# Optimization experiments

Measured on AMD Instinct MI355X. Metric: run time of the kernel, lower is better.

Reference implementation:

```python
import jax, jax.numpy as jnp
import numpy as np

HIDDEN = 4096
HALF = HIDDEN // 2
NUM_EXPERTS = 64
TOP_K = 8
TEMPERATURE = 1.0


def setup_inputs() -> dict:
    key = jax.random.key(0)
    k_x, k_w1, k_w2 = jax.random.split(key, 3)
    B, S = 4, 4096
    x = jax.random.normal(k_x, (B, S, HIDDEN), dtype=jnp.float32)
    attention_mask = jnp.ones((B, S), dtype=jnp.float32)
    # nn.init.normal_(std=0.02), zero bias
    W1 = 0.02 * jax.random.normal(k_w1, (HIDDEN, HALF), dtype=jnp.float32)
    b1 = jnp.zeros((HALF,), dtype=jnp.float32)
    W2 = 0.02 * jax.random.normal(k_w2, (HALF, NUM_EXPERTS), dtype=jnp.float32)
    b2 = jnp.zeros((NUM_EXPERTS,), dtype=jnp.float32)
    return {"x": x, "attention_mask": attention_mask, "W1": W1, "b1": b1, "W2": W2, "b2": b2}


def reference(x, attention_mask, W1, b1, W2, b2):
    B, S, H = x.shape
    x_flat = x.reshape(-1, H)  # [T, H], T = B*S
    # router MLP (eval mode: dropout is identity, no noise)
    h = jax.nn.gelu(x_flat @ W1 + b1, approximate=False)  # [T, H/2]
    logits = h @ W2 + b2  # [T, E]
    T = logits.shape[0]
    # top-k sparse gating: softmax over selected logits, scatter into dense [T, E]
    top_v, top_i = jax.lax.top_k(logits, TOP_K)  # [T, K]
    top_w = jax.nn.softmax(top_v / TEMPERATURE, axis=-1)  # [T, K]
    weights = jnp.zeros_like(logits).at[jnp.arange(T)[:, None], top_i].set(top_w)
    expert_weights = weights.reshape(B, S, NUM_EXPERTS)
    router_logits = logits.reshape(B, S, NUM_EXPERTS)
    mask = attention_mask[:, :, None].astype(expert_weights.dtype)
    expert_weights = expert_weights * mask
    router_logits = router_logits * mask
    return expert_weights, router_logits
```

## Files before the change

kernel.cpp:

```cpp
#include <hip/hip_runtime.h>
#include <hip/hip_bf16.h>
#include <math.h>

#define HIDDEN 4096
#define HALF   2048
#define NE     64
#define TOPK   8

typedef __attribute__((ext_vector_type(8))) short          short8;
typedef __attribute__((ext_vector_type(4))) float          floatx4;
typedef __attribute__((ext_vector_type(4))) unsigned short ushort4v;

__device__ inline unsigned short bf16_rne(float v) {
    union { float f; unsigned u; } x; x.f = v;
    unsigned r = x.u + 0x7fffu + ((x.u >> 16) & 1u);
    return (unsigned short)(r >> 16);
}
__device__ inline float bf16_to_f(unsigned short b) {
    union { unsigned u; float f; } x; x.u = (unsigned)b << 16;
    return x.f;
}

__device__ inline void hstore(float* p, float v) { *p = v; }
__device__ inline void hstore(__hip_bfloat16* p, float v) { *p = __float2bfloat16(v); }
__device__ inline float hload(const float* p) { return *p; }
__device__ inline float hload(const __hip_bfloat16* p) { return __bfloat162float(*p); }
__device__ inline float ntload(const float* p) { return __builtin_nontemporal_load(p); }
__device__ inline float ntload(const __hip_bfloat16* p) { return __bfloat162float(*p); }

__device__ inline void gl2lds16(const void* g, void* l) {
    __builtin_amdgcn_global_load_lds(
        (const __attribute__((address_space(1))) void*)g,
        (__attribute__((address_space(3))) void*)l, 16, 0, 0);
}

__global__ __launch_bounds__(256) void split_x_k(const float* __restrict__ x,
                                                 unsigned short* __restrict__ hi,
                                                 unsigned short* __restrict__ lo) {
    const size_t blk = (size_t)(gridDim.x - 1 - blockIdx.x);
    const size_t i = (blk * 256 + threadIdx.x) * 4;
    floatx4 v = __builtin_nontemporal_load((const floatx4*)(x + i));
    ushort4v h4, l4;
#pragma unroll
    for (int j = 0; j < 4; ++j) {
        unsigned short hb = bf16_rne(v[j]);
        h4[j] = hb;
        l4[j] = bf16_rne(v[j] - bf16_to_f(hb));
    }
    *(ushort4v*)(hi + i) = h4;
    *(ushort4v*)(lo + i) = l4;
}

__global__ __launch_bounds__(256) void split_wt_k(const float* __restrict__ src,
                                                  unsigned short* __restrict__ wh,
                                                  unsigned short* __restrict__ wl,
                                                  int K, int N) {
    __shared__ float tile[64][65];
    const int tid = threadIdx.x;
    const int bk = blockIdx.x * 64, bn = blockIdx.y * 64;
    const int c4 = (tid & 15) * 4, r = tid >> 4;
#pragma unroll
    for (int rr = 0; rr < 4; ++rr) {
        const int row = r + rr * 16;
        *(float4*)&tile[row][c4] = *(const float4*)&src[(size_t)(bk + row) * N + bn + c4];
    }
    __syncthreads();
#pragma unroll
    for (int rr = 0; rr < 4; ++rr) {
        const int n = r + rr * 16;
        ushort4v h4, l4;
#pragma unroll
        for (int j = 0; j < 4; ++j) {
            float v = tile[c4 + j][n];
            unsigned short hb = bf16_rne(v);
            h4[j] = hb;
            l4[j] = bf16_rne(v - bf16_to_f(hb));
        }
        *(ushort4v*)&wh[(size_t)(bn + n) * K + bk + c4] = h4;
        *(ushort4v*)&wl[(size_t)(bn + n) * K + bk + c4] = l4;
    }
}

__global__ __launch_bounds__(256, 2) void gemm1_gelu_pre(const unsigned short* __restrict__ xh,
                                                         const unsigned short* __restrict__ xl,
                                                         const unsigned short* __restrict__ wh,
                                                         const unsigned short* __restrict__ wl,
                                                         const float* __restrict__ bias1,
                                                         float* __restrict__ h) {
    __shared__ unsigned short Ah[2][128][32];
    __shared__ unsigned short Al[2][128][32];
    __shared__ unsigned short Bh[2][128][32];
    __shared__ unsigned short Bl[2][128][32];

    const int tid = threadIdx.x;
    const int id  = blockIdx.x;
    const int c   = id >> 9;
    const int j   = id & 511;
    const int m0  = ((c << 5) | (j >> 4)) * 128;
    const int N0  = (j & 15) * 128;

    const int wave = tid >> 6, lane = tid & 63;
    const int wm   = (wave & 1) * 64;
    const int wn   = (wave >> 1) * 64;
    const int l15  = lane & 15;
    const int q    = lane >> 4;

    const size_t lrow = (size_t)(lane >> 2);
    const int    lcol = (lane & 3) * 8;
    const unsigned short* gp;
    unsigned short* lp;
    if (wave == 0)      { gp = xh + (m0 + lrow) * HIDDEN + lcol; lp = &Ah[0][0][0]; }
    else if (wave == 1) { gp = xl + (m0 + lrow) * HIDDEN + lcol; lp = &Al[0][0][0]; }
    else if (wave == 2) { gp = wh + (N0 + lrow) * HIDDEN + lcol; lp = &Bh[0][0][0]; }
    else                { gp = wl + (N0 + lrow) * HIDDEN + lcol; lp = &Bl[0][0][0]; }

    float bb[4];
#pragma unroll
    for (int jj = 0; jj < 4; ++jj) bb[jj] = bias1[N0 + wn + jj * 16 + l15];
    asm volatile("s_waitcnt vmcnt(0)" ::: "memory");

    const unsigned aoff = ((unsigned)(wm + l15)) * 64 + ((unsigned)q) * 16;
    const unsigned boff = ((unsigned)(wn + l15)) * 64 + ((unsigned)q) * 16;
    const char* AhB = (const char*)&Ah[0][0][0];
    const char* AlB = (const char*)&Al[0][0][0];
    const char* BhB = (const char*)&Bh[0][0][0];
    const char* BlB = (const char*)&Bl[0][0][0];

    floatx4 acc[4][4];
#pragma unroll
    for (int i = 0; i < 4; ++i)
#pragma unroll
        for (int jj = 0; jj < 4; ++jj) acc[i][jj] = (floatx4)0.f;

#pragma unroll
    for (int s = 0; s < 8; ++s)
        gl2lds16(gp + (size_t)s * 16 * HIDDEN, lp + s * 512);
    gp += 32;

    for (int t = 0; t < 128; ++t) {
        const int cur = t & 1;

        asm volatile("" ::: "memory");
        __builtin_amdgcn_s_barrier();

        if (t < 127) {
            unsigned short* lq = lp + (cur ^ 1) * 4096;
#pragma unroll
            for (int s = 0; s < 8; ++s)
                gl2lds16(gp + (size_t)s * 16 * HIDDEN, lq + s * 512);
            gp += 32;
            asm volatile("s_waitcnt vmcnt(8)" ::: "memory");
        } else {
            asm volatile("s_waitcnt vmcnt(0)" ::: "memory");
        }

        __builtin_amdgcn_s_barrier();
        asm volatile("" ::: "memory");

        const unsigned o = (unsigned)cur * 8192;
        short8 a_hi[4], a_lo[4], b_hi[4], b_lo[4];
#pragma unroll
        for (int tt = 0; tt < 4; ++tt) {
            a_hi[tt] = *(const short8*)(AhB + o + aoff + tt * 1024);
            a_lo[tt] = *(const short8*)(AlB + o + aoff + tt * 1024);
            b_hi[tt] = *(const short8*)(BhB + o + boff + tt * 1024);
            b_lo[tt] = *(const short8*)(BlB + o + boff + tt * 1024);
        }
#pragma unroll
        for (int i = 0; i < 4; ++i)
#pragma unroll
            for (int jj = 0; jj < 4; ++jj) {
                acc[i][jj] = __builtin_amdgcn_mfma_f32_16x16x32_bf16(a_hi[i], b_hi[jj], acc[i][jj], 0, 0, 0);
                acc[i][jj] = __builtin_amdgcn_mfma_f32_16x16x32_bf16(a_lo[i], b_hi[jj], acc[i][jj], 0, 0, 0);
                acc[i][jj] = __builtin_amdgcn_mfma_f32_16x16x32_bf16(a_hi[i], b_lo[jj], acc[i][jj], 0, 0, 0);
            }
    }

#pragma unroll
    for (int jj = 0; jj < 4; ++jj) {
        const int n = N0 + wn + jj * 16 + l15;
#pragma unroll
        for (int i = 0; i < 4; ++i) {
            const int mbase = m0 + wm + i * 16 + q * 4;
#pragma unroll
            for (int r = 0; r < 4; ++r) {
                float v = acc[i][jj][r] + bb[jj];
                float g = 0.5f * v * (1.0f + erff(v * 0.70710678118654752f));
                __builtin_nontemporal_store(g, &h[(size_t)(mbase + r) * HALF + n]);
            }
        }
    }
}

template <typename HT>
__global__ __launch_bounds__(256) void gemm2_topk(const HT* __restrict__ h,
                                                  const float* __restrict__ W2,
                                                  const float* __restrict__ bias2,
                                                  const float* __restrict__ amask,
                                                  float* __restrict__ out, int T) {
    __shared__ float hs[4][HALF];
    __shared__ float red[4][4][NE];
    const int tid = threadIdx.x;
    const size_t r0 = (size_t)blockIdx.x * 4;

    float* hsf = &hs[0][0];
    const HT* hr = h + r0 * HALF;
#pragma unroll
    for (int it = 0; it < 8; ++it) {
        const int i = tid * 4 + it * 1024;
        hsf[i + 0] = ntload(hr + i + 0);
        hsf[i + 1] = ntload(hr + i + 1);
        hsf[i + 2] = ntload(hr + i + 2);
        hsf[i + 3] = ntload(hr + i + 3);
    }
    __syncthreads();

    const int e = tid & 63, qq = tid >> 6;
    float s0 = 0.f, s1 = 0.f, s2 = 0.f, s3 = 0.f;
    const float* w = W2 + e;
    const int kbeg = qq * 512;
    for (int k4 = kbeg; k4 < kbeg + 512; k4 += 4) {
        float4 h0 = *(const float4*)&hs[0][k4];
        float4 h1 = *(const float4*)&hs[1][k4];
        float4 h2 = *(const float4*)&hs[2][k4];
        float4 h3 = *(const float4*)&hs[3][k4];
        float wv;
        wv = w[(size_t)(k4 + 0) * NE];
        s0 = fmaf(h0.x, wv, s0); s1 = fmaf(h1.x, wv, s1); s2 = fmaf(h2.x, wv, s2); s3 = fmaf(h3.x, wv, s3);
        wv = w[(size_t)(k4 + 1) * NE];
        s0 = fmaf(h0.y, wv, s0); s1 = fmaf(h1.y, wv, s1); s2 = fmaf(h2.y, wv, s2); s3 = fmaf(h3.y, wv, s3);
        wv = w[(size_t)(k4 + 2) * NE];
        s0 = fmaf(h0.z, wv, s0); s1 = fmaf(h1.z, wv, s1); s2 = fmaf(h2.z, wv, s2); s3 = fmaf(h3.z, wv, s3);
        wv = w[(size_t)(k4 + 3) * NE];
        s0 = fmaf(h0.w, wv, s0); s1 = fmaf(h1.w, wv, s1); s2 = fmaf(h2.w, wv, s2); s3 = fmaf(h3.w, wv, s3);
    }
    red[qq][0][e] = s0;
    red[qq][1][e] = s1;
    red[qq][2][e] = s2;
    red[qq][3][e] = s3;
    __syncthreads();

    const int wave = tid >> 6, lane = tid & 63;
    const size_t r = r0 + wave;
    const float v = ((red[0][wave][lane] + red[1][wave][lane]) +
                     (red[2][wave][lane] + red[3][wave][lane])) + bias2[lane];
    const float mk = amask[r];

    out[(size_t)T * NE + r * NE + lane] = v * mk;

    bool  sel = false;
    float m0 = 0.f, Z = 0.f;
#pragma unroll
    for (int it = 0; it < TOPK; ++it) {
        float cand = sel ? -INFINITY : v;
        int   idx  = lane;
#pragma unroll
        for (int off = 32; off; off >>= 1) {
            float ov = __shfl_xor(cand, off, 64);
            int   oi = __shfl_xor(idx,  off, 64);
            if (ov > cand || (ov == cand && oi < idx)) { cand = ov; idx = oi; }
        }
        if (it == 0) m0 = cand;
        Z += expf(cand - m0);
        if (lane == idx) sel = true;
    }
    const float wgt = sel ? (expf(v - m0) / Z) : 0.f;
    out[r * NE + lane] = wgt * mk;
}

template <typename HT>
__global__ __launch_bounds__(256, 2) void gemm1_gelu_mfma(const float* __restrict__ x,
                                                          const float* __restrict__ W1,
                                                          const float* __restrict__ bias1,
                                                          HT* __restrict__ h) {
    __shared__ unsigned short Ah[128][40];
    __shared__ unsigned short Al[128][40];
    __shared__ unsigned short Bh[128][40];
    __shared__ unsigned short Bl[128][40];

    const int tid  = threadIdx.x;
    const int m0   = blockIdx.x * 128;
    const int n0   = blockIdx.y * 128;
    const int wave = tid >> 6, lane = tid & 63;
    const int wm   = (wave & 1) * 64;
    const int wn   = (wave >> 1) * 64;
    const int l15  = lane & 15;
    const int q    = lane >> 4;
    const int sm = tid & 127;
    const int kh = (tid >> 7) * 16;

    floatx4 acc[4][4];
#pragma unroll
    for (int i = 0; i < 4; ++i)
#pragma unroll
        for (int j = 0; j < 4; ++j) acc[i][j] = (floatx4)0.f;

    const float* xp = x  + (size_t)(m0 + sm) * HIDDEN + kh;
    const float* wp = W1 + (size_t)kh * HALF + n0 + sm;

    for (int k0 = 0; k0 < HIDDEN; k0 += 32) {
        float4 av[4];
#pragma unroll
        for (int i = 0; i < 4; ++i) av[i] = *(const float4*)(xp + k0 + i * 4);
        float bv[16];
#pragma unroll
        for (int i = 0; i < 16; ++i) bv[i] = wp[(size_t)(k0 + i) * HALF];

        __syncthreads();
        {
            unsigned short hi[16], lo[16];
#pragma unroll
            for (int i = 0; i < 4; ++i) {
                const float vs[4] = {av[i].x, av[i].y, av[i].z, av[i].w};
#pragma unroll
                for (int j = 0; j < 4; ++j) {
                    float v = vs[j];
                    unsigned short hb = bf16_rne(v);
                    hi[i * 4 + j] = hb;
                    lo[i * 4 + j] = bf16_rne(v - bf16_to_f(hb));
                }
            }
            *(short8*)&Ah[sm][kh]     = *(const short8*)&hi[0];
            *(short8*)&Ah[sm][kh + 8] = *(const short8*)&hi[8];
            *(short8*)&Al[sm][kh]     = *(const short8*)&lo[0];
            *(short8*)&Al[sm][kh + 8] = *(const short8*)&lo[8];
        }
        {
            unsigned short hi[16], lo[16];
#pragma unroll
            for (int i = 0; i < 16; ++i) {
                float v = bv[i];
                unsigned short hb = bf16_rne(v);
                hi[i] = hb;
                lo[i] = bf16_rne(v - bf16_to_f(hb));
            }
            *(short8*)&Bh[sm][kh]     = *(const short8*)&hi[0];
            *(short8*)&Bh[sm][kh + 8] = *(const short8*)&hi[8];
            *(short8*)&Bl[sm][kh]     = *(const short8*)&lo[0];
            *(short8*)&Bl[sm][kh + 8] = *(const short8*)&lo[8];
        }
        __syncthreads();

        short8 a_hi[4], a_lo[4], b_hi[4], b_lo[4];
#pragma unroll
        for (int t = 0; t < 4; ++t) {
            a_hi[t] = *(const short8*)&Ah[wm + t * 16 + l15][q * 8];
            a_lo[t] = *(const short8*)&Al[wm + t * 16 + l15][q * 8];
            b_hi[t] = *(const short8*)&Bh[wn + t * 16 + l15][q * 8];
            b_lo[t] = *(const short8*)&Bl[wn + t * 16 + l15][q * 8];
        }
#pragma unroll
        for (int i = 0; i < 4; ++i)
#pragma unroll
            for (int j = 0; j < 4; ++j) {
                acc[i][j] = __builtin_amdgcn_mfma_f32_16x16x32_bf16(a_hi[i], b_hi[j], acc[i][j], 0, 0, 0);
                acc[i][j] = __builtin_amdgcn_mfma_f32_16x16x32_bf16(a_lo[i], b_hi[j], acc[i][j], 0, 0, 0);
                acc[i][j] = __builtin_amdgcn_mfma_f32_16x16x32_bf16(a_hi[i], b_lo[j], acc[i][j], 0, 0, 0);
            }
    }

#pragma unroll
    for (int j = 0; j < 4; ++j) {
        const int n = n0 + wn + j * 16 + l15;
        const float bb = bias1[n];
#pragma unroll
        for (int i = 0; i < 4; ++i) {
            const int mbase = m0 + wm + i * 16 + q * 4;
#pragma unroll
            for (int r = 0; r < 4; ++r) {
                float v = acc[i][j][r] + bb;
                float g = 0.5f * v * (1.0f + erff(v * 0.70710678118654752f));
                hstore(h + (size_t)(mbase + r) * HALF + n, g);
            }
        }
    }
}

extern "C" void kernel_launch(void* const* d_in, const int* in_sizes, int n_in,
                              void* d_out, int out_size, void* d_ws, size_t ws_size,
                              hipStream_t stream) {
    const float* x   = (const float*)d_in[0];
    const float* am  = (const float*)d_in[1];
    const float* W1  = (const float*)d_in[2];
    const float* b1  = (const float*)d_in[3];
    const float* W2  = (const float*)d_in[4];
    const float* b2  = (const float*)d_in[5];
    float* out = (float*)d_out;

    const int T = in_sizes[0] / HIDDEN;

    const size_t h32_bytes     = (size_t)T * HALF * sizeof(float);
    const size_t xsplit_bytes  = (size_t)T * HIDDEN * 2;
    const size_t w1split_bytes = (size_t)HIDDEN * HALF * 2;
    const size_t need_new = h32_bytes + 2 * xsplit_bytes + 2 * w1split_bytes;

    if (ws_size >= need_new) {
        char* p = (char*)d_ws;
        float* h = (float*)p;                     p += h32_bytes;
        unsigned short* xhp = (unsigned short*)p; p += xsplit_bytes;
        unsigned short* xlp = (unsigned short*)p; p += xsplit_bytes;
        unsigned short* w1h = (unsigned short*)p; p += w1split_bytes;
        unsigned short* w1l = (unsigned short*)p;

        const size_t xN = (size_t)T * HIDDEN;
        hipLaunchKernelGGL(split_x_k, dim3(xN / (4 * 256)), dim3(256), 0, stream, x, xhp, xlp);
        hipLaunchKernelGGL(split_wt_k, dim3(HIDDEN / 64, HALF / 64), dim3(256), 0, stream,
                           W1, w1h, w1l, HIDDEN, HALF);
        hipLaunchKernelGGL(gemm1_gelu_pre, dim3((T / 128) * (HALF / 128)), dim3(256), 0, stream,
                           xhp, xlp, w1h, w1l, b1, h);
        hipLaunchKernelGGL((gemm2_topk<float>), dim3(T / 4), dim3(256), 0, stream,
                           h, W2, b2, am, out, T);
    } else if (ws_size >= h32_bytes) {
        float* h = (float*)d_ws;
        hipLaunchKernelGGL((gemm1_gelu_mfma<float>), dim3(T / 128, HALF / 128), dim3(256), 0, stream,
                           x, W1, b1, h);
        hipLaunchKernelGGL((gemm2_topk<float>), dim3(T / 4), dim3(256), 0, stream,
                           h, W2, b2, am, out, T);
    } else {
        __hip_bfloat16* h = (__hip_bfloat16*)d_ws;
        hipLaunchKernelGGL((gemm1_gelu_mfma<__hip_bfloat16>), dim3(T / 128, HALF / 128), dim3(256), 0, stream,
                           x, W1, b1, h);
        hipLaunchKernelGGL((gemm2_topk<__hip_bfloat16>), dim3(T / 4), dim3(256), 0, stream,
                           h, W2, b2, am, out, T);
    }
}
```

Before: 1.330 ms.

## Load W1 split fragments directly from global, stage only X in LDS

The GEMM1 kernel stops staging the B (W1 hi/lo) tiles through LDS. Each wave now reads its MFMA B fragments straight from global memory, and LDS holds only the A (x hi/lo) double buffer. All four waves share the A loads, and launch bounds go from 2 to 3 blocks per CU to use the freed LDS. The split_x kernel now handles 8 elements per thread with 16-byte nontemporal stores. The direct B loads are synchronous global reads inside the loop with no prefetch, so memory latency may be exposed and per-wave traffic for W rises.

```diff
diff --git a/kernel.cpp b/kernel.cpp
--- a/kernel.cpp
+++ b/kernel.cpp
@@ -38,17 +38,24 @@
                                                  unsigned short* __restrict__ hi,
                                                  unsigned short* __restrict__ lo) {
     const size_t blk = (size_t)(gridDim.x - 1 - blockIdx.x);
-    const size_t i = (blk * 256 + threadIdx.x) * 4;
-    floatx4 v = __builtin_nontemporal_load((const floatx4*)(x + i));
-    ushort4v h4, l4;
+    const size_t i = (blk * 256 + threadIdx.x) * 8;
+    floatx4 v0 = __builtin_nontemporal_load((const floatx4*)(x + i));
+    floatx4 v1 = __builtin_nontemporal_load((const floatx4*)(x + i + 4));
+    short8 h8, l8;
 #pragma unroll
     for (int j = 0; j < 4; ++j) {
-        unsigned short hb = bf16_rne(v[j]);
-        h4[j] = hb;
-        l4[j] = bf16_rne(v[j] - bf16_to_f(hb));
-    }
-    *(ushort4v*)(hi + i) = h4;
-    *(ushort4v*)(lo + i) = l4;
+        unsigned short hb = bf16_rne(v0[j]);
+        h8[j] = (short)hb;
+        l8[j] = (short)bf16_rne(v0[j] - bf16_to_f(hb));
+    }
+#pragma unroll
+    for (int j = 0; j < 4; ++j) {
+        unsigned short hb = bf16_rne(v1[j]);
+        h8[4 + j] = (short)hb;
+        l8[4 + j] = (short)bf16_rne(v1[j] - bf16_to_f(hb));
+    }
+    __builtin_nontemporal_store(h8, (short8*)(hi + i));
+    __builtin_nontemporal_store(l8, (short8*)(lo + i));
 }
 
 __global__ __launch_bounds__(256) void split_wt_k(const float* __restrict__ src,
@@ -81,7 +88,7 @@
     }
 }
 
-__global__ __launch_bounds__(256, 2) void gemm1_gelu_pre(const unsigned short* __restrict__ xh,
+__global__ __launch_bounds__(256, 3) void gemm1_gelu_pre(const unsigned short* __restrict__ xh,
                                                          const unsigned short* __restrict__ xl,
                                                          const unsigned short* __restrict__ wh,
                                                          const unsigned short* __restrict__ wl,
@@ -89,8 +96,6 @@
                                                          float* __restrict__ h) {
     __shared__ unsigned short Ah[2][128][32];
     __shared__ unsigned short Al[2][128][32];
-    __shared__ unsigned short Bh[2][128][32];
-    __shared__ unsigned short Bl[2][128][32];
 
     const int tid = threadIdx.x;
     const int id  = blockIdx.x;
@@ -107,12 +112,14 @@
 
     const size_t lrow = (size_t)(lane >> 2);
     const int    lcol = (lane & 3) * 8;
-    const unsigned short* gp;
-    unsigned short* lp;
-    if (wave == 0)      { gp = xh + (m0 + lrow) * HIDDEN + lcol; lp = &Ah[0][0][0]; }
-    else if (wave == 1) { gp = xl + (m0 + lrow) * HIDDEN + lcol; lp = &Al[0][0][0]; }
-    else if (wave == 2) { gp = wh + (N0 + lrow) * HIDDEN + lcol; lp = &Bh[0][0][0]; }
-    else                { gp = wl + (N0 + lrow) * HIDDEN + lcol; lp = &Bl[0][0][0]; }
+    const int    rbase = (wave & 1) * 64;
+    const unsigned short* gp =
+        ((wave & 2) ? xl : xh) + (size_t)(m0 + rbase + lrow) * HIDDEN + lcol;
+    unsigned short* lp =
+        ((wave & 2) ? &Al[0][0][0] : &Ah[0][0][0]) + rbase * 32;
+
+    const unsigned short* bph = wh + (size_t)(N0 + wn + l15) * HIDDEN + q * 8;
+    const unsigned short* bpl = wl + (size_t)(N0 + wn + l15) * HIDDEN + q * 8;
 
     float bb[4];
 #pragma unroll
@@ -120,11 +127,8 @@
     asm volatile("s_waitcnt vmcnt(0)" ::: "memory");
 
     const unsigned aoff = ((unsigned)(wm + l15)) * 64 + ((unsigned)q) * 16;
-    const unsigned boff = ((unsigned)(wn + l15)) * 64 + ((unsigned)q) * 16;
     const char* AhB = (const char*)&Ah[0][0][0];
     const char* AlB = (const char*)&Al[0][0][0];
-    const char* BhB = (const char*)&Bh[0][0][0];
-    const char* BlB = (const char*)&Bl[0][0][0];
 
     floatx4 acc[4][4];
 #pragma unroll
@@ -133,7 +137,7 @@
         for (int jj = 0; jj < 4; ++jj) acc[i][jj] = (floatx4)0.f;
 
 #pragma unroll
-    for (int s = 0; s < 8; ++s)
+    for (int s = 0; s < 4; ++s)
         gl2lds16(gp + (size_t)s * 16 * HIDDEN, lp + s * 512);
     gp += 32;
 
@@ -146,10 +150,10 @@
         if (t < 127) {
             unsigned short* lq = lp + (cur ^ 1) * 4096;
 #pragma unroll
-            for (int s = 0; s < 8; ++s)
+            for (int s = 0; s < 4; ++s)
                 gl2lds16(gp + (size_t)s * 16 * HIDDEN, lq + s * 512);
             gp += 32;
-            asm volatile("s_waitcnt vmcnt(8)" ::: "memory");
+            asm volatile("s_waitcnt vmcnt(4)" ::: "memory");
         } else {
             asm volatile("s_waitcnt vmcnt(0)" ::: "memory");
         }
@@ -157,14 +161,21 @@
         __builtin_amdgcn_s_barrier();
         asm volatile("" ::: "memory");
 
+        short8 b_hi[4], b_lo[4];
+#pragma unroll
+        for (int tt = 0; tt < 4; ++tt) {
+            b_hi[tt] = *(const short8*)(bph + (size_t)tt * 16 * HIDDEN);
+            b_lo[tt] = *(const short8*)(bpl + (size_t)tt * 16 * HIDDEN);
+        }
+        bph += 32;
+        bpl += 32;
+
         const unsigned o = (unsigned)cur * 8192;
-        short8 a_hi[4], a_lo[4], b_hi[4], b_lo[4];
+        short8 a_hi[4], a_lo[4];
 #pragma unroll
         for (int tt = 0; tt < 4; ++tt) {
             a_hi[tt] = *(const short8*)(AhB + o + aoff + tt * 1024);
             a_lo[tt] = *(const short8*)(AlB + o + aoff + tt * 1024);
-            b_hi[tt] = *(const short8*)(BhB + o + boff + tt * 1024);
-            b_lo[tt] = *(const short8*)(BlB + o + boff + tt * 1024);
         }
 #pragma unroll
         for (int i = 0; i < 4; ++i)
@@ -403,7 +414,7 @@
         unsigned short* w1l = (unsigned short*)p;
 
         const size_t xN = (size_t)T * HIDDEN;
-        hipLaunchKernelGGL(split_x_k, dim3(xN / (4 * 256)), dim3(256), 0, stream, x, xhp, xlp);
+        hipLaunchKernelGGL(split_x_k, dim3(xN / (8 * 256)), dim3(256), 0, stream, x, xhp, xlp);
         hipLaunchKernelGGL(split_wt_k, dim3(HIDDEN / 64, HALF / 64), dim3(256), 0, stream,
                            W1, w1h, w1l, HIDDEN, HALF);
         hipLaunchKernelGGL(gemm1_gelu_pre, dim3((T / 128) * (HALF / 128)), dim3(256), 0, stream,
```

Measured after the change: 1.680 ms. 1.26x slower.
